# Kernel tuning notes

Hardware: AMD Instinct MI355X
Metric: run time of the kernel (lower is better)

## Reference

```python
import jax, jax.numpy as jnp
import numpy as np

B, N, IN_DIM, ATT_DIM = 2, 8192, 512, 512


def setup_inputs() -> dict:
    key = jax.random.key(0)
    k1, k2, k3, k4 = jax.random.split(key, 4)
    X = jax.random.normal(k1, (B, N, IN_DIM), dtype=jnp.float32)
    adj = jax.random.uniform(k2, (B, N, N), dtype=jnp.float32)
    mask = jnp.ones((B, N), dtype=jnp.float32)
    # Learned params (torch Linear stores W as (out,in); we store (in,out) for x @ W)
    Wqk = jax.random.normal(k3, (IN_DIM, 2 * ATT_DIM), dtype=jnp.float32) / np.sqrt(IN_DIM)
    Wv = jax.random.normal(k4, (IN_DIM, IN_DIM), dtype=jnp.float32) / np.sqrt(IN_DIM)
    return {"X": X, "adj": adj, "mask": mask, "Wqk": Wqk, "Wv": Wv}


def reference(X, adj, mask, Wqk, Wv):
    # q, k: (B, N, att_dim); v: (B, N, in_dim)
    qk = X @ Wqk
    q, k = jnp.split(qk, 2, axis=-1)
    v = X @ Wv
    att_dim = q.shape[-1]
    inv_scale = 1.0 / jnp.sqrt(jnp.float32(att_dim))
    # Original math: w_i = inv_scale * sum_j adj_ij * m_i * m_j * (q_i . k_j).
    # Since the rank-1 mask factors (m_i m_j), fold m_j into k and m_i into the row
    # score, avoiding a second materialized NxN tensor:
    k_m = k * mask[:, :, None]                       # (B, N, att_dim)
    agg = jnp.einsum("bij,bjd->bid", adj, k_m)       # (B, N, att_dim)
    w = inv_scale * mask * jnp.einsum("bid,bid->bi", q, agg)  # (B, N)
    # softmax over the bag dimension (dim=1), then scale v rows
    L = jax.nn.softmax(w, axis=1)[:, :, None] * v    # (B, N, in_dim)
    return L
```

## Files before the change

kernel.cpp:

```cpp
#include <hip/hip_runtime.h>
#include <math.h>

#define BB 2
#define NN 8192
#define DD 512

static const float INV_SCALE = 0.04419417382415922f;

typedef short s16x8 __attribute__((ext_vector_type(8)));
typedef unsigned short u16x8 __attribute__((ext_vector_type(8)));
typedef float f32x4 __attribute__((ext_vector_type(4)));

#define AS1 __attribute__((address_space(1)))
#define AS3 __attribute__((address_space(3)))

__device__ __forceinline__ unsigned short bfbits(__bf16 h) {
    return __builtin_bit_cast(unsigned short, h);
}

__device__ __forceinline__ void gll16(const void* g, void* l) {
    __builtin_amdgcn_global_load_lds((const AS1 unsigned int*)g, (AS3 unsigned int*)l, 16, 0, 0);
}

__global__ __launch_bounds__(256) void convx_k(
    const float* __restrict__ X, unsigned short* __restrict__ Xhi,
    unsigned short* __restrict__ Xlo)
{
    long i = (long)blockIdx.x * 256 + threadIdx.x;
    float4 x = ((const float4*)X)[i];
    __bf16 h0 = (__bf16)x.x, h1 = (__bf16)x.y, h2 = (__bf16)x.z, h3 = (__bf16)x.w;
    ushort4 hi4 = make_ushort4(bfbits(h0), bfbits(h1), bfbits(h2), bfbits(h3));
    __bf16 l0 = (__bf16)(x.x - (float)h0), l1 = (__bf16)(x.y - (float)h1);
    __bf16 l2 = (__bf16)(x.z - (float)h2), l3 = (__bf16)(x.w - (float)h3);
    ushort4 lo4 = make_ushort4(bfbits(l0), bfbits(l1), bfbits(l2), bfbits(l3));
    ((ushort4*)Xhi)[i] = hi4;
    ((ushort4*)Xlo)[i] = lo4;
}

__global__ __launch_bounds__(256) void convw_k(
    const float* __restrict__ Wqk, const float* __restrict__ Wv,
    unsigned short* __restrict__ QTh, unsigned short* __restrict__ QTl,
    unsigned short* __restrict__ VTh, unsigned short* __restrict__ VTl)
{
    int i = blockIdx.x * 256 + threadIdx.x;
    float val; unsigned short *ph, *pl;
    if (i < 524288) {
        int n = i >> 9, k = i & 511;
        val = Wqk[k * 1024 + n]; ph = QTh + i; pl = QTl + i;
    } else {
        int o = i - 524288; int n = o >> 9, k = o & 511;
        val = Wv[k * 512 + n]; ph = VTh + o; pl = VTl + o;
    }
    __bf16 h = (__bf16)val;
    __bf16 l = (__bf16)(val - (float)h);
    *ph = bfbits(h); *pl = bfbits(l);
}

template <int EPI, int NT>
__global__ __launch_bounds__(256, 2) void mfma_gemm(
    const unsigned short* __restrict__ A0, const unsigned short* __restrict__ A1,
    const unsigned short* __restrict__ B0, const unsigned short* __restrict__ B1,
    float* __restrict__ C,
    float* __restrict__ q, float* __restrict__ km,
    unsigned short* __restrict__ kmT, const float* __restrict__ mask,
    int N, int K)
{
    constexpr int BK = 32;
    constexpr int TILE_SH = 128 * BK;

    __shared__ unsigned short Asm[2 * TILE_SH];
    __shared__ unsigned short Bsm[2 * TILE_SH];

    const int t = threadIdx.x;
    const int wv = t >> 6, lane = t & 63;
    const int wm = wv >> 1, wn = wv & 1;
    const long m0 = blockIdx.x * 128;
    const int n0 = blockIdx.y * 128;

    f32x4 acc[4][4];
#pragma unroll
    for (int i = 0; i < 4; ++i)
#pragma unroll
        for (int j = 0; j < 4; ++j) acc[i][j] = {0.f, 0.f, 0.f, 0.f};

    const int swzcol = ((lane & 3) ^ ((lane >> 2) & 3)) * 16;
    auto stageA16 = [&](int term, int k0, int buf) {
        const unsigned short* Ab = (term < 2) ? A0 : A1;
#pragma unroll
        for (int u = 0; u < 2; ++u) {
            int c = wv * 2 + u;
            int row = c * 16 + (lane >> 2);
            gll16((const char*)Ab + ((m0 + row) * (long)K + k0) * 2 + swzcol,
                  (char*)Asm + buf * (TILE_SH * 2) + c * 1024);
        }
    };
    auto stageB16 = [&](int term, int k0, int buf) {
        const unsigned short* Bb = (NT == 3 && term == 1) ? B1 : B0;
#pragma unroll
        for (int u = 0; u < 2; ++u) {
            int c = wv * 2 + u;
            int row = c * 16 + (lane >> 2);
            gll16((const char*)Bb + ((long)(n0 + row) * K + k0) * 2 + swzcol,
                  (char*)Bsm + buf * (TILE_SH * 2) + c * 1024);
        }
    };

    stageA16(0, 0, 0);
    stageB16(0, 0, 0);
    __syncthreads();

    const int NTILES = NT * (K / BK);
    int cur = 0, term = 0, k0 = 0;
    const int g = lane >> 4;

#pragma unroll 2
    for (int tt = 0; tt < NTILES; ++tt) {
        int k0n = k0 + BK, termn = term;
        if (k0n == K) { k0n = 0; ++termn; }
        const bool hasNext = (tt + 1 < NTILES);

        if (hasNext) {
            stageA16(termn, k0n, cur ^ 1);
            stageB16(termn, k0n, cur ^ 1);
        }

        s16x8 av[4], bv[4];
#pragma unroll
        for (int f = 0; f < 4; ++f) {
            int ra = wm * 64 + f * 16 + (lane & 15);
            int rb = wn * 64 + f * 16 + (lane & 15);
            av[f] = *(const s16x8*)(Asm + cur * TILE_SH + ra * BK + ((g ^ (ra & 3)) << 3));
            bv[f] = *(const s16x8*)(Bsm + cur * TILE_SH + rb * BK + ((g ^ (rb & 3)) << 3));
        }
#pragma unroll
        for (int fm = 0; fm < 4; ++fm)
#pragma unroll
            for (int fn = 0; fn < 4; ++fn)
                acc[fm][fn] = __builtin_amdgcn_mfma_f32_16x16x32_bf16(
                    av[fm], bv[fn], acc[fm][fn], 0, 0, 0);

        __syncthreads();
        cur ^= 1; term = termn; k0 = k0n;
    }

    const long rbase = m0 + wm * 64;
    const int cbase = n0 + wn * 64;

    if constexpr (EPI == 0) {
#pragma unroll
        for (int fm = 0; fm < 4; ++fm) {
            long rb = rbase + fm * 16 + ((lane >> 4) << 2);
#pragma unroll
            for (int fn = 0; fn < 4; ++fn) {
                int c = cbase + fn * 16 + (lane & 15);
#pragma unroll
                for (int j = 0; j < 4; ++j)
                    C[(rb + j) * (long)N + c] = acc[fm][fn][j];
            }
        }
    } else {
        const bool isq = (n0 < 512);
#pragma unroll
        for (int fm = 0; fm < 4; ++fm) {
            long rb = rbase + fm * 16 + ((lane >> 4) << 2);
#pragma unroll
            for (int fn = 0; fn < 4; ++fn) {
                int c = cbase + fn * 16 + (lane & 15);
                if (isq) {
#pragma unroll
                    for (int j = 0; j < 4; ++j)
                        q[(rb + j) * 512L + c] = acc[fm][fn][j];
                } else {
                    int c2 = c - 512;
                    float kv[4];
#pragma unroll
                    for (int j = 0; j < 4; ++j) {
                        kv[j] = acc[fm][fn][j] * mask[rb + j];
                        km[(rb + j) * 512L + c2] = kv[j];
                    }
                    ushort4 pk = make_ushort4(bfbits((__bf16)kv[0]), bfbits((__bf16)kv[1]),
                                              bfbits((__bf16)kv[2]), bfbits((__bf16)kv[3]));
                    long b = rb >> 13, r = rb & 8191;
                    *(ushort4*)(kmT + (b << 22) + ((long)c2 << 13) + r) = pk;
                }
            }
        }
    }
}

__global__ __launch_bounds__(512, 1) void adj_gemm(
    const float* __restrict__ adj,
    const unsigned short* __restrict__ kmT,
    const float* __restrict__ q,
    float* __restrict__ w)
{
    constexpr int NT = NN / 64;
    __shared__ unsigned short Asm[2 * 64 * 64];
    __shared__ unsigned short Bsm[2 * 512 * 64];

    const int t = threadIdx.x;
    const int wv = t >> 6, lane = t & 63;

    const int bid = (int)blockIdx.x;
    const int lid = (bid & 7) * 32 + (bid >> 3);
    const int x = lid & 127, z = lid >> 7;
    const long m0 = (long)x * 64;

    const float* Az = adj + (long)z * NN * NN;
    const unsigned short* Bz = kmT + ((long)z << 22);

    f32x4 acc[4][4];
#pragma unroll
    for (int i = 0; i < 4; ++i)
#pragma unroll
        for (int j = 0; j < 4; ++j) acc[i][j] = {0.f, 0.f, 0.f, 0.f};

    const int bswz = ((lane & 7) ^ (lane >> 3)) << 4;
    auto stageB = [&](int tt, int buf) {
        const long k0 = (long)tt * 64;
#pragma unroll
        for (int u = 0; u < 8; ++u) {
            int c = wv * 8 + u;
            int d = c * 8 + (lane >> 3);
            gll16((const char*)Bz + ((long)d * NN + k0) * 2 + bswz,
                  (char*)Bsm + buf * 65536 + c * 1024);
        }
    };

    const int arow = t >> 3;
    const int ac8  = t & 7;
    auto issueA = [&](int tt, float4 (&r)[2]) {
        const float* s = Az + (m0 + arow) * (long)NN + (long)tt * 64 + ac8 * 8;
        r[0] = *(const float4*)s;
        r[1] = *(const float4*)(s + 4);
    };
    auto commitA = [&](float4 (&r)[2], int buf) {
        float4 a = r[0], b = r[1];
        u16x8 pk;
        pk[0] = bfbits((__bf16)a.x); pk[1] = bfbits((__bf16)a.y);
        pk[2] = bfbits((__bf16)a.z); pk[3] = bfbits((__bf16)a.w);
        pk[4] = bfbits((__bf16)b.x); pk[5] = bfbits((__bf16)b.y);
        pk[6] = bfbits((__bf16)b.z); pk[7] = bfbits((__bf16)b.w);
        *(u16x8*)(Asm + buf * 4096 + arow * 64 + ((ac8 ^ (arow & 7)) << 3)) = pk;
    };

    const int g = lane >> 4;
    auto compute = [&](int buf) {
#pragma unroll
        for (int ks = 0; ks < 2; ++ks) {
            s16x8 av[4], bv[4];
#pragma unroll
            for (int f = 0; f < 4; ++f) {
                int ma = f * 16 + (lane & 15);
                int nb = wv * 64 + f * 16 + (lane & 15);
                av[f] = *(const s16x8*)(Asm + buf * 4096 + ma * 64
                         + (((g + ks * 4) ^ (ma & 7)) << 3));
                bv[f] = *(const s16x8*)(Bsm + buf * 32768 + nb * 64
                         + (((g + ks * 4) ^ (nb & 7)) << 3));
            }
#pragma unroll
            for (int fm = 0; fm < 4; ++fm)
#pragma unroll
                for (int fn = 0; fn < 4; ++fn)
                    acc[fm][fn] = __builtin_amdgcn_mfma_f32_16x16x32_bf16(
                        av[fm], bv[fn], acc[fm][fn], 0, 0, 0);
        }
    };

    float4 rA[2];
    issueA(0, rA);
    stageB(0, 0);
    commitA(rA, 0);
    __syncthreads();

#pragma unroll 2
    for (int tt = 0; tt < NT; ++tt) {
        const int cur = tt & 1;
        const bool hasNext = (tt + 1 < NT);
        if (hasNext) {
            issueA(tt + 1, rA);
            stageB(tt + 1, cur ^ 1);
        }
        compute(cur);
        if (hasNext) commitA(rA, cur ^ 1);
        __syncthreads();
    }

    const long zrow = (long)z * NN;
#pragma unroll
    for (int fm = 0; fm < 4; ++fm) {
#pragma unroll
        for (int j = 0; j < 4; ++j) {
            long r = zrow + m0 + fm * 16 + ((lane >> 4) << 2) + j;
            const float* qr = q + r * 512L + wv * 64 + (lane & 15);
            float s = 0.f;
#pragma unroll
            for (int fn = 0; fn < 4; ++fn)
                s += qr[fn * 16] * acc[fm][fn][j];
            s += __shfl_xor(s, 1); s += __shfl_xor(s, 2);
            s += __shfl_xor(s, 4); s += __shfl_xor(s, 8);
            if ((lane & 15) == 0) atomicAdd(w + r, s);
        }
    }
}

__global__ __launch_bounds__(256) void fixup_k(
    float* __restrict__ w, const float* __restrict__ mask)
{
    int i = blockIdx.x * 256 + threadIdx.x;
    w[i] *= INV_SCALE * mask[i];
}

__global__ __launch_bounds__(256) void wmax_k(const float* __restrict__ w,
                                              float* __restrict__ wmax)
{
    const int b = blockIdx.x;
    const float* wr = w + (long)b * NN;
    const int t = threadIdx.x;
    float m = -3.4e38f;
    for (int i = t; i < NN; i += 256) m = fmaxf(m, wr[i]);
#pragma unroll
    for (int o = 32; o > 0; o >>= 1) m = fmaxf(m, __shfl_down(m, o));
    __shared__ float red[4];
    if ((t & 63) == 0) red[t >> 6] = m;
    __syncthreads();
    if (t == 0) wmax[b] = fmaxf(fmaxf(red[0], red[1]), fmaxf(red[2], red[3]));
}

__global__ __launch_bounds__(256) void select_k(
    const float* __restrict__ w, const float* __restrict__ wmax,
    int* __restrict__ count, int* __restrict__ cand)
{
    int i = blockIdx.x * 256 + threadIdx.x;
    int b = i >> 13;
    if (w[i] >= wmax[b] - 15.f) {
        int p = atomicAdd(count, 1);
        if (p < 128) cand[p] = i;
    }
}

__global__ __launch_bounds__(256) void refine_k(
    const float* __restrict__ q, const float* __restrict__ km,
    const float* __restrict__ adj, const int* __restrict__ cand,
    const int* __restrict__ count, float* __restrict__ partial)
{
    int y = blockIdx.y;
    int cnt = *count; if (cnt > 128) cnt = 128;
    if (y >= cnt) return;
    const int row = cand[y];
    const int b = row >> 13, r = row & 8191;
    const int x = blockIdx.x;
    const int t = threadIdx.x, w = t >> 6, l = t & 63;

    const float* qr = q + (long)row * 512 + l * 8;
    const float4 q0 = *(const float4*)qr;
    const float4 q1 = *(const float4*)(qr + 4);
    const float* kmB = km + ((long)b << 13) * 512;
    const float* adjR = adj + (((long)b << 13) + r) * 8192L;

    float acc = 0.f;
    const int jbase = x * 128 + w * 32;
    for (int i = 0; i < 32; ++i) {
        int j = jbase + i;
        const float* kr = kmB + (long)j * 512 + l * 8;
        const float4 k0 = *(const float4*)kr;
        const float4 k1 = *(const float4*)(kr + 4);
        float d = q0.x * k0.x + q0.y * k0.y + q0.z * k0.z + q0.w * k0.w
                + q1.x * k1.x + q1.y * k1.y + q1.z * k1.z + q1.w * k1.w;
#pragma unroll
        for (int o = 32; o > 0; o >>= 1) d += __shfl_down(d, o);
        if (l == 0) acc += adjR[j] * d;
    }
    __shared__ float red[4];
    if (l == 0) red[w] = acc;
    __syncthreads();
    if (t == 0) partial[y * 64 + x] = red[0] + red[1] + red[2] + red[3];
}

__global__ __launch_bounds__(128) void apply_k(
    const int* __restrict__ cand, const int* __restrict__ count,
    const float* __restrict__ partial, const float* __restrict__ mask,
    float* __restrict__ w)
{
    int t = threadIdx.x;
    int cnt = *count; if (cnt > 128) cnt = 128;
    if (t < cnt) {
        float s = 0.f;
        for (int x = 0; x < 64; ++x) s += partial[t * 64 + x];
        int row = cand[t];
        w[row] = s * INV_SCALE * mask[row];
    }
}

__global__ __launch_bounds__(1024) void softmax_k(
    const float* __restrict__ w, float* __restrict__ p)
{
    const int b = blockIdx.x;
    const float* wr = w + (long)b * NN;
    float* pr = p + (long)b * NN;
    const int t = threadIdx.x;
    __shared__ float red[16];
    __shared__ float bmax, bsum;

    float m = -3.4e38f;
    for (int i = t; i < NN; i += 1024) m = fmaxf(m, wr[i]);
#pragma unroll
    for (int o = 32; o > 0; o >>= 1) m = fmaxf(m, __shfl_down(m, o));
    if ((t & 63) == 0) red[t >> 6] = m;
    __syncthreads();
    if (t == 0) {
        float mm = red[0];
        for (int i = 1; i < 16; ++i) mm = fmaxf(mm, red[i]);
        bmax = mm;
    }
    __syncthreads();
    const float M = bmax;

    float s = 0.f;
    for (int i = t; i < NN; i += 1024) s += expf(wr[i] - M);
#pragma unroll
    for (int o = 32; o > 0; o >>= 1) s += __shfl_down(s, o);
    __syncthreads();
    if ((t & 63) == 0) red[t >> 6] = s;
    __syncthreads();
    if (t == 0) {
        float ss = 0.f;
        for (int i = 0; i < 16; ++i) ss += red[i];
        bsum = ss;
    }
    __syncthreads();
    const float invS = 1.f / bsum;
    for (int i = t; i < NN; i += 1024) pr[i] = expf(wr[i] - M) * invS;
}

__global__ __launch_bounds__(256) void scale_k(
    const float* __restrict__ v, const float* __restrict__ p,
    float* __restrict__ out)
{
    const long i = (long)blockIdx.x * 256 + threadIdx.x;
    const int row = (int)(i >> 7);
    const float pv = p[row];
    float4 vv = ((const float4*)v)[i];
    vv.x *= pv; vv.y *= pv; vv.z *= pv; vv.w *= pv;
    ((float4*)out)[i] = vv;
}

extern "C" void kernel_launch(void* const* d_in, const int* in_sizes, int n_in,
                              void* d_out, int out_size, void* d_ws, size_t ws_size,
                              hipStream_t stream)
{
    const float* X    = (const float*)d_in[0];
    const float* adj  = (const float*)d_in[1];
    const float* mask = (const float*)d_in[2];
    const float* Wqk  = (const float*)d_in[3];
    const float* Wv   = (const float*)d_in[4];
    float* out = (float*)d_out;

    char* ws = (char*)d_ws;
    const long SZB = 33554432;
    float* q_buf  = (float*)(ws);
    float* km_buf = (float*)(ws + SZB);
    float* v_buf  = (float*)(ws + 2 * SZB);
    unsigned short* Xhi = (unsigned short*)(ws + 3 * SZB);
    unsigned short* Xlo = Xhi + 8388608;
    unsigned short* kmT = (unsigned short*)(ws + 4 * SZB);
    unsigned short* QTh = (unsigned short*)(ws + 4 * SZB + 16777216);
    unsigned short* QTl = QTh + 524288;
    unsigned short* VTh = QTl + 524288;
    unsigned short* VTl = VTh + 262144;
    float* w_buf = (float*)(VTl + 262144);
    float* p_buf = w_buf + 16384;
    float* wmax  = p_buf + 16384;
    float* partial = wmax + 64;
    int* count = (int*)(partial + 8192);
    int* cand  = count + 64;

    hipMemsetAsync(count, 0, 4, stream);
    hipMemsetAsync(w_buf, 0, 16384 * 4, stream);

    convx_k<<<8192, 256, 0, stream>>>(X, Xhi, Xlo);
    convw_k<<<3072, 256, 0, stream>>>(Wqk, Wv, QTh, QTl, VTh, VTl);

    mfma_gemm<1, 3><<<dim3(128, 8, 1), 256, 0, stream>>>(
        Xhi, Xlo, QTh, QTl, nullptr, q_buf, km_buf, kmT, mask, 1024, 512);

    mfma_gemm<0, 1><<<dim3(128, 4, 1), 256, 0, stream>>>(
        Xhi, nullptr, VTh, nullptr, v_buf, nullptr, nullptr, nullptr, nullptr,
        512, 512);

    adj_gemm<<<256, 512, 0, stream>>>(adj, kmT, q_buf, w_buf);

    fixup_k<<<64, 256, 0, stream>>>(w_buf, mask);

    wmax_k<<<BB, 256, 0, stream>>>(w_buf, wmax);
    select_k<<<64, 256, 0, stream>>>(w_buf, wmax, count, cand);
    refine_k<<<dim3(64, 128, 1), 256, 0, stream>>>(q_buf, km_buf, adj, cand, count, partial);
    apply_k<<<1, 128, 0, stream>>>(cand, count, partial, mask, w_buf);

    softmax_k<<<BB, 1024, 0, stream>>>(w_buf, p_buf);
    scale_k<<<8192, 256, 0, stream>>>(v_buf, p_buf, out);
}
```

Baseline: 474.4 us.

## Reassociate attention score as q·kmᵀ GEMM with fused adj-weighted row reduction

```diff
diff --git a/kernel.cpp b/kernel.cpp
--- a/kernel.cpp
+++ b/kernel.cpp
@@ -62,8 +62,8 @@
     const unsigned short* __restrict__ B0, const unsigned short* __restrict__ B1,
     float* __restrict__ C,
     float* __restrict__ q, float* __restrict__ km,
-    unsigned short* __restrict__ kmT, const float* __restrict__ mask,
-    int N, int K)
+    unsigned short* __restrict__ qh, unsigned short* __restrict__ kmh,
+    const float* __restrict__ mask, int N, int K)
 {
     constexpr int BK = 32;
     constexpr int TILE_SH = 128 * BK;
@@ -168,46 +168,44 @@
                 int c = cbase + fn * 16 + (lane & 15);
                 if (isq) {
 #pragma unroll
-                    for (int j = 0; j < 4; ++j)
-                        q[(rb + j) * 512L + c] = acc[fm][fn][j];
+                    for (int j = 0; j < 4; ++j) {
+                        float val = acc[fm][fn][j];
+                        q [(rb + j) * 512L + c] = val;
+                        qh[(rb + j) * 512L + c] = bfbits((__bf16)val);
+                    }
                 } else {
                     int c2 = c - 512;
-                    float kv[4];
 #pragma unroll
                     for (int j = 0; j < 4; ++j) {
-                        kv[j] = acc[fm][fn][j] * mask[rb + j];
-                        km[(rb + j) * 512L + c2] = kv[j];
+                        float kv = acc[fm][fn][j] * mask[rb + j];
+                        km [(rb + j) * 512L + c2] = kv;
+                        kmh[(rb + j) * 512L + c2] = bfbits((__bf16)kv);
                     }
-                    ushort4 pk = make_ushort4(bfbits((__bf16)kv[0]), bfbits((__bf16)kv[1]),
-                                              bfbits((__bf16)kv[2]), bfbits((__bf16)kv[3]));
-                    long b = rb >> 13, r = rb & 8191;
-                    *(ushort4*)(kmT + (b << 22) + ((long)c2 << 13) + r) = pk;
                 }
             }
         }
     }
 }
 
-__global__ __launch_bounds__(512, 1) void adj_gemm(
+__global__ __launch_bounds__(256, 4) void sq_gemm(
+    const unsigned short* __restrict__ qh,
+    const unsigned short* __restrict__ kmh,
     const float* __restrict__ adj,
-    const unsigned short* __restrict__ kmT,
-    const float* __restrict__ q,
     float* __restrict__ w)
 {
-    constexpr int NT = NN / 64;
-    __shared__ unsigned short Asm[2 * 64 * 64];
-    __shared__ unsigned short Bsm[2 * 512 * 64];
+    constexpr int BK = 32;
+    constexpr int TILE_SH = 128 * BK;
+
+    __shared__ unsigned short Asm[2 * TILE_SH];
+    __shared__ unsigned short Bsm[2 * TILE_SH];
 
     const int t = threadIdx.x;
     const int wv = t >> 6, lane = t & 63;
-
-    const int bid = (int)blockIdx.x;
-    const int lid = (bid & 7) * 32 + (bid >> 3);
-    const int x = lid & 127, z = lid >> 7;
-    const long m0 = (long)x * 64;
-
-    const float* Az = adj + (long)z * NN * NN;
-    const unsigned short* Bz = kmT + ((long)z << 22);
+    const int wm = wv >> 1, wn = wv & 1;
+    const int z = blockIdx.z;
+    const long m0 = (long)z * NN + blockIdx.x * 128;
+    const int n0 = blockIdx.y * 128;
+    const unsigned short* Bz = kmh + (long)z * NN * 512;
 
     f32x4 acc[4][4];
 #pragma unroll
@@ -215,91 +213,74 @@
 #pragma unroll
         for (int j = 0; j < 4; ++j) acc[i][j] = {0.f, 0.f, 0.f, 0.f};
 
-    const int bswz = ((lane & 7) ^ (lane >> 3)) << 4;
-    auto stageB = [&](int tt, int buf) {
-        const long k0 = (long)tt * 64;
-#pragma unroll
-        for (int u = 0; u < 8; ++u) {
-            int c = wv * 8 + u;
-            int d = c * 8 + (lane >> 3);
-            gll16((const char*)Bz + ((long)d * NN + k0) * 2 + bswz,
-                  (char*)Bsm + buf * 65536 + c * 1024);
+    const int swzcol = ((lane & 3) ^ ((lane >> 2) & 3)) * 16;
+    auto stageA = [&](int k0, int buf) {
+#pragma unroll
+        for (int u = 0; u < 2; ++u) {
+            int c = wv * 2 + u;
+            int row = c * 16 + (lane >> 2);
+            gll16((const char*)qh + ((m0 + row) * 512L + k0) * 2 + swzcol,
+                  (char*)Asm + buf * (TILE_SH * 2) + c * 1024);
         }
     };
-
-    const int arow = t >> 3;
-    const int ac8  = t & 7;
-    auto issueA = [&](int tt, float4 (&r)[2]) {
-        const float* s = Az + (m0 + arow) * (long)NN + (long)tt * 64 + ac8 * 8;
-        r[0] = *(const float4*)s;
-        r[1] = *(const float4*)(s + 4);
+    auto stageB = [&](int k0, int buf) {
+#pragma unroll
+        for (int u = 0; u < 2; ++u) {
+            int c = wv * 2 + u;
+            int row = c * 16 + (lane >> 2);
+            gll16((const char*)Bz + ((long)(n0 + row) * 512 + k0) * 2 + swzcol,
+                  (char*)Bsm + buf * (TILE_SH * 2) + c * 1024);
+        }
     };
-    auto commitA = [&](float4 (&r)[2], int buf) {
-        float4 a = r[0], b = r[1];
-        u16x8 pk;
-        pk[0] = bfbits((__bf16)a.x); pk[1] = bfbits((__bf16)a.y);
-        pk[2] = bfbits((__bf16)a.z); pk[3] = bfbits((__bf16)a.w);
-        pk[4] = bfbits((__bf16)b.x); pk[5] = bfbits((__bf16)b.y);
-        pk[6] = bfbits((__bf16)b.z); pk[7] = bfbits((__bf16)b.w);
-        *(u16x8*)(Asm + buf * 4096 + arow * 64 + ((ac8 ^ (arow & 7)) << 3)) = pk;
-    };
+
+    stageA(0, 0);
+    stageB(0, 0);
+    __syncthreads();
 
     const int g = lane >> 4;
-    auto compute = [&](int buf) {
-#pragma unroll
-        for (int ks = 0; ks < 2; ++ks) {
-            s16x8 av[4], bv[4];
-#pragma unroll
-            for (int f = 0; f < 4; ++f) {
-                int ma = f * 16 + (lane & 15);
-                int nb = wv * 64 + f * 16 + (lane & 15);
-                av[f] = *(const s16x8*)(Asm + buf * 4096 + ma * 64
-                         + (((g + ks * 4) ^ (ma & 7)) << 3));
-                bv[f] = *(const s16x8*)(Bsm + buf * 32768 + nb * 64
-                         + (((g + ks * 4) ^ (nb & 7)) << 3));
-            }
-#pragma unroll
-            for (int fm = 0; fm < 4; ++fm)
-#pragma unroll
-                for (int fn = 0; fn < 4; ++fn)
-                    acc[fm][fn] = __builtin_amdgcn_mfma_f32_16x16x32_bf16(
-                        av[fm], bv[fn], acc[fm][fn], 0, 0, 0);
-        }
-    };
-
-    float4 rA[2];
-    issueA(0, rA);
-    stageB(0, 0);
-    commitA(rA, 0);
-    __syncthreads();
-
 #pragma unroll 2
-    for (int tt = 0; tt < NT; ++tt) {
+    for (int tt = 0; tt < 16; ++tt) {
         const int cur = tt & 1;
-        const bool hasNext = (tt + 1 < NT);
+        const bool hasNext = (tt + 1 < 16);
         if (hasNext) {
-            issueA(tt + 1, rA);
-            stageB(tt + 1, cur ^ 1);
-        }
-        compute(cur);
-        if (hasNext) commitA(rA, cur ^ 1);
+            stageA((tt + 1) * BK, cur ^ 1);
+            stageB((tt + 1) * BK, cur ^ 1);
+        }
+
+        s16x8 av[4], bv[4];
+#pragma unroll
+        for (int f = 0; f < 4; ++f) {
+            int ra = wm * 64 + f * 16 + (lane & 15);
+            int rb = wn * 64 + f * 16 + (lane & 15);
+            av[f] = *(const s16x8*)(Asm + cur * TILE_SH + ra * BK + ((g ^ (ra & 3)) << 3));
+            bv[f] = *(const s16x8*)(Bsm + cur * TILE_SH + rb * BK + ((g ^ (rb & 3)) << 3));
+        }
+#pragma unroll
+        for (int fm = 0; fm < 4; ++fm)
+#pragma unroll
+            for (int fn = 0; fn < 4; ++fn)
+                acc[fm][fn] = __builtin_amdgcn_mfma_f32_16x16x32_bf16(
+                    av[fm], bv[fn], acc[fm][fn], 0, 0, 0);
+
         __syncthreads();
     }
 
-    const long zrow = (long)z * NN;
+    const float* adjZ = adj + (long)z * NN * NN;
+    const int libase = blockIdx.x * 128 + wm * 64;
+    const int jbase = n0 + wn * 64;
 #pragma unroll
     for (int fm = 0; fm < 4; ++fm) {
 #pragma unroll
         for (int j = 0; j < 4; ++j) {
-            long r = zrow + m0 + fm * 16 + ((lane >> 4) << 2) + j;
-            const float* qr = q + r * 512L + wv * 64 + (lane & 15);
+            int li = libase + fm * 16 + ((lane >> 4) << 2) + j;
+            const float* ar = adjZ + (long)li * NN + jbase + (lane & 15);
             float s = 0.f;
 #pragma unroll
             for (int fn = 0; fn < 4; ++fn)
-                s += qr[fn * 16] * acc[fm][fn][j];
+                s += ar[fn * 16] * acc[fm][fn][j];
             s += __shfl_xor(s, 1); s += __shfl_xor(s, 2);
             s += __shfl_xor(s, 4); s += __shfl_xor(s, 8);
-            if ((lane & 15) == 0) atomicAdd(w + r, s);
+            if ((lane & 15) == 0) atomicAdd(w + (long)z * NN + li, s);
         }
     }
 }
@@ -463,8 +444,9 @@
     float* v_buf  = (float*)(ws + 2 * SZB);
     unsigned short* Xhi = (unsigned short*)(ws + 3 * SZB);
     unsigned short* Xlo = Xhi + 8388608;
-    unsigned short* kmT = (unsigned short*)(ws + 4 * SZB);
-    unsigned short* QTh = (unsigned short*)(ws + 4 * SZB + 16777216);
+    unsigned short* qh  = (unsigned short*)(ws + 4 * SZB);
+    unsigned short* kmh = qh + 8388608;
+    unsigned short* QTh = kmh + 8388608;
     unsigned short* QTl = QTh + 524288;
     unsigned short* VTh = QTl + 524288;
     unsigned short* VTl = VTh + 262144;
@@ -482,13 +464,13 @@
     convw_k<<<3072, 256, 0, stream>>>(Wqk, Wv, QTh, QTl, VTh, VTl);
 
     mfma_gemm<1, 3><<<dim3(128, 8, 1), 256, 0, stream>>>(
-        Xhi, Xlo, QTh, QTl, nullptr, q_buf, km_buf, kmT, mask, 1024, 512);
+        Xhi, Xlo, QTh, QTl, nullptr, q_buf, km_buf, qh, kmh, mask, 1024, 512);
 
     mfma_gemm<0, 1><<<dim3(128, 4, 1), 256, 0, stream>>>(
         Xhi, nullptr, VTh, nullptr, v_buf, nullptr, nullptr, nullptr, nullptr,
-        512, 512);
-
-    adj_gemm<<<256, 512, 0, stream>>>(adj, kmT, q_buf, w_buf);
+        nullptr, 512, 512);
+
+    sq_gemm<<<dim3(64, 64, 2), 256, 0, stream>>>(qh, kmh, adj, w_buf);
 
     fixup_k<<<64, 256, 0, stream>>>(w_buf, mask);
 
```

Result: faster. 463.3 us (-2.3%).
